# Kernel optimization log

Hardware: AMD Instinct MI355X
Metric: run time of the kernel (lower is better)

## Reference

```python
import jax, jax.numpy as jnp
import numpy as np

PATCH, STRIDE, NUM_PROJ, NBINS = 7, 1, 16, 2 ** 16
B, C, H, W = 2, 3, 384, 384


def gaussian_kernel(size=7, sigma=1.2):
    x = jnp.arange(size, dtype=jnp.float32)
    # faithful to original: exp(...)**2 (square applied OUTSIDE the exp)
    return jnp.exp((x - size // 2) ** 2 / (-2.0 * sigma ** 2)) ** 2


def extract_patches(img, p, s):
    # Equivalent of F.unfold: [b, c, h, w] -> [b, N, c*p*p], torch channel-major feature order
    b, c, h, w = img.shape
    Ho = (h - p) // s + 1
    Wo = (w - p) // s + 1
    cols = [img[:, :, i:i + (Ho - 1) * s + 1:s, j:j + (Wo - 1) * s + 1:s]
            for i in range(p) for j in range(p)]
    pat = jnp.stack(cols, axis=2)  # [b, c, p*p, Ho, Wo]
    return pat.reshape(b, c * p * p, Ho * Wo).transpose(0, 2, 1)  # [b, N, c*p*p]


def hist_distance(px, py):
    # px, py: [N] projected values for one (batch, projection) pair
    min_v = jnp.minimum(py.min(), px.min())
    max_v = jnp.maximum(py.max(), px.max())
    scale = max_v - min_v
    # scatter-set 1s into a 65536-bin histogram at data-dependent indices
    y_idx = jnp.floor((NBINS - 1) * (py - min_v) / scale).astype(jnp.int32)
    y_hist = jnp.zeros((NBINS,), jnp.float32).at[y_idx].set(1.0)
    # valid conv1d with 7-tap gaussian (symmetric kernel, so corr == conv)
    y_hist = jnp.convolve(y_hist, gaussian_kernel(), mode='valid')  # [NBINS-6]
    y_hist = jnp.minimum(y_hist, 1.0)
    Wd = y_hist.shape[0]
    # grid_sample (bilinear, align_corners=False, zero padding) on a 1-tall image == 1D linear interp
    gx = 2.0 * (px - min_v) / scale - 1.0
    ix = ((gx + 1.0) * Wd - 1.0) / 2.0
    x0 = jnp.floor(ix)
    w1 = ix - x0
    x0i = x0.astype(jnp.int32)
    x1i = x0i + 1
    v0 = jnp.where((x0i >= 0) & (x0i < Wd), y_hist[jnp.clip(x0i, 0, Wd - 1)], 0.0)
    v1 = jnp.where((x1i >= 0) & (x1i < Wd), y_hist[jnp.clip(x1i, 0, Wd - 1)], 0.0)
    return -(v0 * (1.0 - w1) + v1 * w1).sum()


def setup_inputs() -> dict:
    key = jax.random.key(0)
    k1, k2, k3 = jax.random.split(key, 3)
    x = jax.random.normal(k1, (B, C, H, W), dtype=jnp.float32)
    y = jax.random.normal(k2, (B, C, H, W), dtype=jnp.float32)
    rand = jax.random.normal(k3, (B, C * PATCH * PATCH, NUM_PROJ), dtype=jnp.float32)
    return {"x": x, "y": y, "rand": rand}


def reference(x, y, rand):
    xp = extract_patches(x, PATCH, STRIDE)  # [b, N, d]
    yp = extract_patches(y, PATCH, STRIDE)
    # torch.std(dim=0) is unbiased (ddof=1)
    r = rand / jnp.std(rand, axis=1, keepdims=True, ddof=1)  # [b, d, P]
    proj_x = jnp.einsum('bnd,bdp->bpn', xp, r)
    proj_y = jnp.einsum('bnd,bdp->bpn', yp, r)
    losses = jax.vmap(jax.vmap(hist_distance))(proj_x, proj_y)  # [b, P]
    per_image = losses.sum(axis=1) / NUM_PROJ
    return per_image.mean()  # batch_reduction='mean'
```

## Files before the change

### kernel.cpp

```cpp
#include <hip/hip_runtime.h>
#include <math.h>
#include <stdint.h>

#define NPROJ 16
#define NBINS 65536
#define WD (NBINS - 6)
#define HB 65560
#define B_ 2
#define C_ 3
#define H_ 384
#define W_ 384
#define HO 378
#define NPAT (HO * HO)
#define DF 147
#define BP 32
#define TSTR 24

__device__ inline unsigned f2key(float f) {
    unsigned u = __float_as_uint(f);
    return (u & 0x80000000u) ? ~u : (u | 0x80000000u);
}
__device__ inline float key2f(unsigned k) {
    unsigned u = (k & 0x80000000u) ? (k ^ 0x80000000u) : ~k;
    return __uint_as_float(u);
}

__global__ __launch_bounds__(64) void k_rnorm(const float* __restrict__ rnd,
                                              float* __restrict__ rnorm,
                                              unsigned* __restrict__ keys,
                                              float* __restrict__ out) {
    int bp = blockIdx.x;
    int b = bp / NPROJ, p = bp % NPROJ;
    int lane = threadIdx.x;
    if (lane == 0) {
        keys[2 * bp] = 0xFFFFFFFFu;
        keys[2 * bp + 1] = 0u;
        if (bp == 0) out[0] = 0.f;
    }
    float s = 0.f, s2 = 0.f;
    for (int d = lane; d < DF; d += 64) {
        float v = rnd[((size_t)b * DF + d) * NPROJ + p];
        s += v; s2 += v * v;
    }
    for (int o = 32; o > 0; o >>= 1) { s += __shfl_down(s, o); s2 += __shfl_down(s2, o); }
    s = __shfl(s, 0); s2 = __shfl(s2, 0);
    float mean = s / (float)DF;
    float var = (s2 - (float)DF * mean * mean) / (float)(DF - 1);
    float inv = 1.0f / sqrtf(var);
    for (int d = lane; d < DF; d += 64) {
        size_t idx = ((size_t)b * DF + d) * NPROJ + p;
        rnorm[idx] = rnd[idx] * inv;
    }
}

#define T1H 32
#define T1W 16
__global__ __launch_bounds__(256) void k_projmm(const float* __restrict__ ximg,
                                                const float* __restrict__ yimg,
                                                const float* __restrict__ rnorm,
                                                float* __restrict__ py,
                                                unsigned* __restrict__ keys) {
    __shared__ float tile[C_][T1H + 6][TSTR];
    __shared__ float red_mn[4][NPROJ], red_mx[4][NPROJ];
    int bz = blockIdx.z;
    int b = bz >> 1, isy = bz & 1;
    const float* img = isy ? yimg : ximg;
    int tid = threadIdx.x;
    int tx = tid & 15, ty = tid >> 4;
    int h0 = blockIdx.y * T1H, w0 = blockIdx.x * T1W;

    for (int c = 0; c < C_; c++)
        for (int i = tid; i < (T1H + 6) * (T1W + 6); i += 256) {
            int r = i / (T1W + 6), col = i % (T1W + 6);
            int h = h0 + r, w = w0 + col;
            tile[c][r][col] = (h < H_ && w < W_)
                ? img[((size_t)(b * C_ + c) * H_ + h) * W_ + w] : 0.f;
        }
    __syncthreads();

    const float* wbase = rnorm + (size_t)b * DF * NPROJ;

    float acc[2][NPROJ];
#pragma unroll
    for (int q = 0; q < 2; q++)
#pragma unroll
        for (int p = 0; p < NPROJ; p++) acc[q][p] = 0.f;

    for (int c = 0; c < C_; c++)
        for (int i = 0; i < 7; i++)
#pragma unroll
            for (int j = 0; j < 7; j++) {
                const float* wrow = wbase + (c * 49 + i * 7 + j) * NPROJ;
                float wv[NPROJ];
#pragma unroll
                for (int p = 0; p < NPROJ; p++) wv[p] = wrow[p];
                float pix0 = tile[c][ty + i][tx + j];
                float pix1 = tile[c][ty + 16 + i][tx + j];
#pragma unroll
                for (int p = 0; p < NPROJ; p++) {
                    acc[0][p] = fmaf(pix0, wv[p], acc[0][p]);
                    acc[1][p] = fmaf(pix1, wv[p], acc[1][p]);
                }
            }

    int wo = w0 + tx;
    int ho0 = h0 + ty, ho1 = h0 + ty + 16;
    bool vm0 = (ho0 < HO) && (wo < HO);
    bool vm1 = (ho1 < HO) && (wo < HO);

    if (isy) {
        if (vm0) {
            size_t n = (size_t)ho0 * HO + wo;
#pragma unroll
            for (int p = 0; p < NPROJ; p++)
                py[((size_t)(b * NPROJ + p)) * NPAT + n] = acc[0][p];
        }
        if (vm1) {
            size_t n = (size_t)ho1 * HO + wo;
#pragma unroll
            for (int p = 0; p < NPROJ; p++)
                py[((size_t)(b * NPROJ + p)) * NPAT + n] = acc[1][p];
        }
    }

    float pmn[NPROJ], pmx[NPROJ];
#pragma unroll
    for (int p = 0; p < NPROJ; p++) {
        float mn = INFINITY, mx = -INFINITY;
        if (vm0) { mn = acc[0][p]; mx = acc[0][p]; }
        if (vm1) { mn = fminf(mn, acc[1][p]); mx = fmaxf(mx, acc[1][p]); }
        pmn[p] = mn; pmx[p] = mx;
    }
#pragma unroll
    for (int o = 1; o < 64; o <<= 1) {
#pragma unroll
        for (int p = 0; p < NPROJ; p++) {
            pmn[p] = fminf(pmn[p], __shfl_xor(pmn[p], o));
            pmx[p] = fmaxf(pmx[p], __shfl_xor(pmx[p], o));
        }
    }
    int wv4 = tid >> 6;
    if ((tid & 63) == 0) {
#pragma unroll
        for (int p = 0; p < NPROJ; p++) { red_mn[wv4][p] = pmn[p]; red_mx[wv4][p] = pmx[p]; }
    }
    __syncthreads();
    if (tid < NPROJ) {
        float mn = fminf(fminf(red_mn[0][tid], red_mn[1][tid]),
                         fminf(red_mn[2][tid], red_mn[3][tid]));
        float mx = fmaxf(fmaxf(red_mx[0][tid], red_mx[1][tid]),
                         fmaxf(red_mx[2][tid], red_mx[3][tid]));
        atomicMin(&keys[2 * (b * NPROJ + tid)], f2key(mn));
        atomicMax(&keys[2 * (b * NPROJ + tid) + 1], f2key(mx));
    }
}

__global__ __launch_bounds__(256) void k_scatter(const float* __restrict__ py,
                                                 const unsigned* __restrict__ keys,
                                                 uint8_t* __restrict__ hist8) {
    int bp = blockIdx.y;
    float mn = key2f(keys[2 * bp]);
    float sc = key2f(keys[2 * bp + 1]) - mn;
    const float4* src = (const float4*)(py + (size_t)bp * NPAT);
    uint8_t* h = hist8 + (size_t)bp * HB + 8;
    const int n4 = NPAT / 4;
    for (int i = blockIdx.x * blockDim.x + threadIdx.x; i < n4;
         i += gridDim.x * blockDim.x) {
        float4 v = src[i];
        int i0 = (int)floorf(65535.f * (v.x - mn) / sc);
        int i1 = (int)floorf(65535.f * (v.y - mn) / sc);
        int i2 = (int)floorf(65535.f * (v.z - mn) / sc);
        int i3 = (int)floorf(65535.f * (v.w - mn) / sc);
        h[min(max(i0, 0), 65535)] = 1;
        h[min(max(i1, 0), 65535)] = 1;
        h[min(max(i2, 0), 65535)] = 1;
        h[min(max(i3, 0), 65535)] = 1;
    }
}

#define T3 16
__global__ __launch_bounds__(256) void k_projgather(const float* __restrict__ ximg,
                                                    const float* __restrict__ rnorm,
                                                    const unsigned* __restrict__ keys,
                                                    const uint8_t* __restrict__ hist8,
                                                    float* __restrict__ out) {
    __shared__ float tile[C_][T3 + 6][TSTR];
    __shared__ float s_mn[NPROJ], s_sc[NPROJ];
    __shared__ float sred[4];
    int b = blockIdx.z;
    int tid = threadIdx.x;
    int tx = tid & 15, ty = tid >> 4;
    int h0 = blockIdx.y * T3, w0 = blockIdx.x * T3;

    if (tid < NPROJ) {
        float mn = key2f(keys[2 * (b * NPROJ + tid)]);
        float mx = key2f(keys[2 * (b * NPROJ + tid) + 1]);
        s_mn[tid] = mn;
        s_sc[tid] = mx - mn;
    }
    for (int c = 0; c < C_; c++)
        for (int i = tid; i < (T3 + 6) * (T3 + 6); i += 256) {
            int r = i / (T3 + 6), col = i % (T3 + 6);
            int h = h0 + r, w = w0 + col;
            tile[c][r][col] = (h < H_ && w < W_)
                ? ximg[((size_t)(b * C_ + c) * H_ + h) * W_ + w] : 0.f;
        }
    __syncthreads();

    const float* wbase = rnorm + (size_t)b * DF * NPROJ;

    float acc[NPROJ];
#pragma unroll
    for (int p = 0; p < NPROJ; p++) acc[p] = 0.f;

    for (int c = 0; c < C_; c++)
        for (int i = 0; i < 7; i++)
#pragma unroll
            for (int j = 0; j < 7; j++) {
                const float* wrow = wbase + (c * 49 + i * 7 + j) * NPROJ;
                float wv[NPROJ];
#pragma unroll
                for (int p = 0; p < NPROJ; p++) wv[p] = wrow[p];
                float pix = tile[c][ty + i][tx + j];
#pragma unroll
                for (int p = 0; p < NPROJ; p++)
                    acc[p] = fmaf(pix, wv[p], acc[p]);
            }

    float g[7];
#pragma unroll
    for (int k = 0; k < 7; k++) {
        float d = (float)(k - 3);
        g[k] = expf(-(d * d) / 1.44f);
    }

    int wo = w0 + tx, ho = h0 + ty;
    float lacc = 0.f;
    if (ho < HO && wo < HO) {
#pragma unroll
        for (int p = 0; p < NPROJ; p++) {
            float v = acc[p];
            float t = (v - s_mn[p]) / s_sc[p];
            float ix = t * (float)WD - 0.5f;
            float x0 = floorf(ix);
            float w1 = ix - x0;
            int x0i = (int)x0;
            int b0 = 8 + x0i;
            int d0 = b0 >> 2, off = b0 & 3;
            const uint32_t* hw =
                (const uint32_t*)(hist8 + (size_t)(b * NPROJ + p) * HB);
            uint32_t u0 = hw[d0], u1 = hw[d0 + 1], u2 = hw[d0 + 2];
            uint64_t lo = (uint64_t)u0 | ((uint64_t)u1 << 32);
            int sh = off * 8;
            uint64_t w8 = (lo >> sh) | ((((uint64_t)u2) << 1) << (63 - sh));
            float f0 = (float)((uint32_t)(w8      ) & 1u);
            float f1 = (float)((uint32_t)(w8 >>  8) & 1u);
            float f2 = (float)((uint32_t)(w8 >> 16) & 1u);
            float f3 = (float)((uint32_t)(w8 >> 24) & 1u);
            float f4 = (float)((uint32_t)(w8 >> 32) & 1u);
            float f5 = (float)((uint32_t)(w8 >> 40) & 1u);
            float f6 = (float)((uint32_t)(w8 >> 48) & 1u);
            float f7 = (float)((uint32_t)(w8 >> 56) & 1u);
            float s0 = g[0] * f0 + g[1] * f1 + g[2] * f2 + g[3] * f3
                     + g[4] * f4 + g[5] * f5 + g[6] * f6;
            float s1 = g[0] * f1 + g[1] * f2 + g[2] * f3 + g[3] * f4
                     + g[4] * f5 + g[5] * f6 + g[6] * f7;
            s0 = fminf(s0, 1.f);
            s1 = fminf(s1, 1.f);
            float r0 = (x0i >= 0) ? s0 : 0.f;
            float r1 = (x0i + 1 < WD) ? s1 : 0.f;
            lacc += r0 * (1.f - w1) + r1 * w1;
        }
    }
    for (int o = 32; o > 0; o >>= 1) lacc += __shfl_down(lacc, o);
    int wv4 = tid >> 6;
    if ((tid & 63) == 0) sred[wv4] = lacc;
    __syncthreads();
    if (tid == 0) {
        float t = sred[0] + sred[1] + sred[2] + sred[3];
        atomicAdd(out, -t * (1.0f / 32.0f));
    }
}

extern "C" void kernel_launch(void* const* d_in, const int* in_sizes, int n_in,
                              void* d_out, int out_size, void* d_ws, size_t ws_size,
                              hipStream_t stream) {
    (void)in_sizes; (void)n_in; (void)out_size; (void)ws_size;
    const float* x = (const float*)d_in[0];
    const float* y = (const float*)d_in[1];
    const float* rnd = (const float*)d_in[2];
    float* out = (float*)d_out;

    float* ws = (float*)d_ws;
    float* rnorm = ws;
    float* py = rnorm + (size_t)B_ * DF * NPROJ;
    unsigned* keys = (unsigned*)(py + (size_t)BP * NPAT);
    uint8_t* hist8 = (uint8_t*)(keys + 2 * BP);

    k_rnorm<<<BP, 64, 0, stream>>>(rnd, rnorm, keys, out);
    hipMemsetAsync(hist8, 0, (size_t)BP * HB, stream);

    dim3 g1(384 / T1W, 384 / T1H, 2 * B_);
    k_projmm<<<g1, 256, 0, stream>>>(x, y, rnorm, py, keys);

    k_scatter<<<dim3(70, BP), 256, 0, stream>>>(py, keys, hist8);

    dim3 g3(384 / T3, 384 / T3, B_);
    k_projgather<<<g3, 256, 0, stream>>>(x, rnorm, keys, hist8, out);
}
```

Baseline: 119.9 us.

## Store x projections once and gather per projection instead of recomputing them

The projection kernel now writes the x projections to workspace along with the y projections, and uses 16x16 tiles with one output per thread. The final kernel no longer recomputes the 147x16 patch projection for x. It streams the stored values per (batch, projection) and looks up a single histogram each, which keeps that histogram's accesses local in cache. The cost is an extra ~9 MB write and read of x projections, and smaller projection tiles, which reduce weight reuse.

```diff
diff --git a/kernel.cpp b/kernel.cpp
--- a/kernel.cpp
+++ b/kernel.cpp
@@ -53,25 +53,26 @@
     }
 }
 
-#define T1H 32
-#define T1W 16
+#define T1 16
 __global__ __launch_bounds__(256) void k_projmm(const float* __restrict__ ximg,
                                                 const float* __restrict__ yimg,
                                                 const float* __restrict__ rnorm,
+                                                float* __restrict__ px,
                                                 float* __restrict__ py,
                                                 unsigned* __restrict__ keys) {
-    __shared__ float tile[C_][T1H + 6][TSTR];
+    __shared__ float tile[C_][T1 + 6][TSTR];
     __shared__ float red_mn[4][NPROJ], red_mx[4][NPROJ];
     int bz = blockIdx.z;
     int b = bz >> 1, isy = bz & 1;
     const float* img = isy ? yimg : ximg;
+    float* proj = isy ? py : px;
     int tid = threadIdx.x;
     int tx = tid & 15, ty = tid >> 4;
-    int h0 = blockIdx.y * T1H, w0 = blockIdx.x * T1W;
+    int h0 = blockIdx.y * T1, w0 = blockIdx.x * T1;
 
     for (int c = 0; c < C_; c++)
-        for (int i = tid; i < (T1H + 6) * (T1W + 6); i += 256) {
-            int r = i / (T1W + 6), col = i % (T1W + 6);
+        for (int i = tid; i < (T1 + 6) * (T1 + 6); i += 256) {
+            int r = i / (T1 + 6), col = i % (T1 + 6);
             int h = h0 + r, w = w0 + col;
             tile[c][r][col] = (h < H_ && w < W_)
                 ? img[((size_t)(b * C_ + c) * H_ + h) * W_ + w] : 0.f;
@@ -80,11 +81,9 @@
 
     const float* wbase = rnorm + (size_t)b * DF * NPROJ;
 
-    float acc[2][NPROJ];
-#pragma unroll
-    for (int q = 0; q < 2; q++)
-#pragma unroll
-        for (int p = 0; p < NPROJ; p++) acc[q][p] = 0.f;
+    float acc[NPROJ];
+#pragma unroll
+    for (int p = 0; p < NPROJ; p++) acc[p] = 0.f;
 
     for (int c = 0; c < C_; c++)
         for (int i = 0; i < 7; i++)
@@ -94,42 +93,27 @@
                 float wv[NPROJ];
 #pragma unroll
                 for (int p = 0; p < NPROJ; p++) wv[p] = wrow[p];
-                float pix0 = tile[c][ty + i][tx + j];
-                float pix1 = tile[c][ty + 16 + i][tx + j];
-#pragma unroll
-                for (int p = 0; p < NPROJ; p++) {
-                    acc[0][p] = fmaf(pix0, wv[p], acc[0][p]);
-                    acc[1][p] = fmaf(pix1, wv[p], acc[1][p]);
-                }
+                float pix = tile[c][ty + i][tx + j];
+#pragma unroll
+                for (int p = 0; p < NPROJ; p++)
+                    acc[p] = fmaf(pix, wv[p], acc[p]);
             }
 
-    int wo = w0 + tx;
-    int ho0 = h0 + ty, ho1 = h0 + ty + 16;
-    bool vm0 = (ho0 < HO) && (wo < HO);
-    bool vm1 = (ho1 < HO) && (wo < HO);
-
-    if (isy) {
-        if (vm0) {
-            size_t n = (size_t)ho0 * HO + wo;
-#pragma unroll
-            for (int p = 0; p < NPROJ; p++)
-                py[((size_t)(b * NPROJ + p)) * NPAT + n] = acc[0][p];
-        }
-        if (vm1) {
-            size_t n = (size_t)ho1 * HO + wo;
-#pragma unroll
-            for (int p = 0; p < NPROJ; p++)
-                py[((size_t)(b * NPROJ + p)) * NPAT + n] = acc[1][p];
-        }
+    int wo = w0 + tx, ho = h0 + ty;
+    bool vm = (ho < HO) && (wo < HO);
+
+    if (vm) {
+        size_t n = (size_t)ho * HO + wo;
+#pragma unroll
+        for (int p = 0; p < NPROJ; p++)
+            proj[((size_t)(b * NPROJ + p)) * NPAT + n] = acc[p];
     }
 
     float pmn[NPROJ], pmx[NPROJ];
 #pragma unroll
     for (int p = 0; p < NPROJ; p++) {
-        float mn = INFINITY, mx = -INFINITY;
-        if (vm0) { mn = acc[0][p]; mx = acc[0][p]; }
-        if (vm1) { mn = fminf(mn, acc[1][p]); mx = fmaxf(mx, acc[1][p]); }
-        pmn[p] = mn; pmx[p] = mx;
+        pmn[p] = vm ? acc[p] : INFINITY;
+        pmx[p] = vm ? acc[p] : -INFINITY;
     }
 #pragma unroll
     for (int o = 1; o < 64; o <<= 1) {
@@ -178,105 +162,69 @@
     }
 }
 
-#define T3 16
-__global__ __launch_bounds__(256) void k_projgather(const float* __restrict__ ximg,
-                                                    const float* __restrict__ rnorm,
-                                                    const unsigned* __restrict__ keys,
-                                                    const uint8_t* __restrict__ hist8,
-                                                    float* __restrict__ out) {
-    __shared__ float tile[C_][T3 + 6][TSTR];
-    __shared__ float s_mn[NPROJ], s_sc[NPROJ];
-    __shared__ float sred[4];
-    int b = blockIdx.z;
-    int tid = threadIdx.x;
-    int tx = tid & 15, ty = tid >> 4;
-    int h0 = blockIdx.y * T3, w0 = blockIdx.x * T3;
-
-    if (tid < NPROJ) {
-        float mn = key2f(keys[2 * (b * NPROJ + tid)]);
-        float mx = key2f(keys[2 * (b * NPROJ + tid) + 1]);
-        s_mn[tid] = mn;
-        s_sc[tid] = mx - mn;
-    }
-    for (int c = 0; c < C_; c++)
-        for (int i = tid; i < (T3 + 6) * (T3 + 6); i += 256) {
-            int r = i / (T3 + 6), col = i % (T3 + 6);
-            int h = h0 + r, w = w0 + col;
-            tile[c][r][col] = (h < H_ && w < W_)
-                ? ximg[((size_t)(b * C_ + c) * H_ + h) * W_ + w] : 0.f;
-        }
-    __syncthreads();
-
-    const float* wbase = rnorm + (size_t)b * DF * NPROJ;
-
-    float acc[NPROJ];
-#pragma unroll
-    for (int p = 0; p < NPROJ; p++) acc[p] = 0.f;
-
-    for (int c = 0; c < C_; c++)
-        for (int i = 0; i < 7; i++)
-#pragma unroll
-            for (int j = 0; j < 7; j++) {
-                const float* wrow = wbase + (c * 49 + i * 7 + j) * NPROJ;
-                float wv[NPROJ];
-#pragma unroll
-                for (int p = 0; p < NPROJ; p++) wv[p] = wrow[p];
-                float pix = tile[c][ty + i][tx + j];
-#pragma unroll
-                for (int p = 0; p < NPROJ; p++)
-                    acc[p] = fmaf(pix, wv[p], acc[p]);
-            }
-
+__device__ inline float gath8(const uint32_t* __restrict__ hw, float v,
+                              float mn, float sc, const float g[7]) {
+    float t = (v - mn) / sc;
+    float ix = t * (float)WD - 0.5f;
+    float x0 = floorf(ix);
+    float w1 = ix - x0;
+    int x0i = (int)x0;
+    int b0 = 8 + x0i;
+    int d0 = b0 >> 2, off = b0 & 3;
+    uint32_t u0 = hw[d0], u1 = hw[d0 + 1], u2 = hw[d0 + 2];
+    uint64_t lo = (uint64_t)u0 | ((uint64_t)u1 << 32);
+    int sh = off * 8;
+    uint64_t w8 = (lo >> sh) | ((((uint64_t)u2) << 1) << (63 - sh));
+    float f0 = (float)((uint32_t)(w8      ) & 1u);
+    float f1 = (float)((uint32_t)(w8 >>  8) & 1u);
+    float f2 = (float)((uint32_t)(w8 >> 16) & 1u);
+    float f3 = (float)((uint32_t)(w8 >> 24) & 1u);
+    float f4 = (float)((uint32_t)(w8 >> 32) & 1u);
+    float f5 = (float)((uint32_t)(w8 >> 40) & 1u);
+    float f6 = (float)((uint32_t)(w8 >> 48) & 1u);
+    float f7 = (float)((uint32_t)(w8 >> 56) & 1u);
+    float s0 = g[0] * f0 + g[1] * f1 + g[2] * f2 + g[3] * f3
+             + g[4] * f4 + g[5] * f5 + g[6] * f6;
+    float s1 = g[0] * f1 + g[1] * f2 + g[2] * f3 + g[3] * f4
+             + g[4] * f5 + g[5] * f6 + g[6] * f7;
+    s0 = fminf(s0, 1.f);
+    s1 = fminf(s1, 1.f);
+    float r0 = (x0i >= 0) ? s0 : 0.f;
+    float r1 = (x0i + 1 < WD) ? s1 : 0.f;
+    return r0 * (1.f - w1) + r1 * w1;
+}
+
+__global__ __launch_bounds__(256) void k_gather8(const float* __restrict__ px,
+                                                 const unsigned* __restrict__ keys,
+                                                 const uint8_t* __restrict__ hist8,
+                                                 float* __restrict__ out) {
+    int bp = blockIdx.y;
+    float mn = key2f(keys[2 * bp]);
+    float sc = key2f(keys[2 * bp + 1]) - mn;
+    const float4* src = (const float4*)(px + (size_t)bp * NPAT);
+    const uint32_t* hw = (const uint32_t*)(hist8 + (size_t)bp * HB);
     float g[7];
 #pragma unroll
     for (int k = 0; k < 7; k++) {
         float d = (float)(k - 3);
         g[k] = expf(-(d * d) / 1.44f);
     }
-
-    int wo = w0 + tx, ho = h0 + ty;
-    float lacc = 0.f;
-    if (ho < HO && wo < HO) {
-#pragma unroll
-        for (int p = 0; p < NPROJ; p++) {
-            float v = acc[p];
-            float t = (v - s_mn[p]) / s_sc[p];
-            float ix = t * (float)WD - 0.5f;
-            float x0 = floorf(ix);
-            float w1 = ix - x0;
-            int x0i = (int)x0;
-            int b0 = 8 + x0i;
-            int d0 = b0 >> 2, off = b0 & 3;
-            const uint32_t* hw =
-                (const uint32_t*)(hist8 + (size_t)(b * NPROJ + p) * HB);
-            uint32_t u0 = hw[d0], u1 = hw[d0 + 1], u2 = hw[d0 + 2];
-            uint64_t lo = (uint64_t)u0 | ((uint64_t)u1 << 32);
-            int sh = off * 8;
-            uint64_t w8 = (lo >> sh) | ((((uint64_t)u2) << 1) << (63 - sh));
-            float f0 = (float)((uint32_t)(w8      ) & 1u);
-            float f1 = (float)((uint32_t)(w8 >>  8) & 1u);
-            float f2 = (float)((uint32_t)(w8 >> 16) & 1u);
-            float f3 = (float)((uint32_t)(w8 >> 24) & 1u);
-            float f4 = (float)((uint32_t)(w8 >> 32) & 1u);
-            float f5 = (float)((uint32_t)(w8 >> 40) & 1u);
-            float f6 = (float)((uint32_t)(w8 >> 48) & 1u);
-            float f7 = (float)((uint32_t)(w8 >> 56) & 1u);
-            float s0 = g[0] * f0 + g[1] * f1 + g[2] * f2 + g[3] * f3
-                     + g[4] * f4 + g[5] * f5 + g[6] * f6;
-            float s1 = g[0] * f1 + g[1] * f2 + g[2] * f3 + g[3] * f4
-                     + g[4] * f5 + g[5] * f6 + g[6] * f7;
-            s0 = fminf(s0, 1.f);
-            s1 = fminf(s1, 1.f);
-            float r0 = (x0i >= 0) ? s0 : 0.f;
-            float r1 = (x0i + 1 < WD) ? s1 : 0.f;
-            lacc += r0 * (1.f - w1) + r1 * w1;
-        }
-    }
-    for (int o = 32; o > 0; o >>= 1) lacc += __shfl_down(lacc, o);
-    int wv4 = tid >> 6;
-    if ((tid & 63) == 0) sred[wv4] = lacc;
+    float acc = 0.f;
+    const int n4 = NPAT / 4;
+    for (int i = blockIdx.x * blockDim.x + threadIdx.x; i < n4;
+         i += gridDim.x * blockDim.x) {
+        float4 v = src[i];
+        acc += gath8(hw, v.x, mn, sc, g);
+        acc += gath8(hw, v.y, mn, sc, g);
+        acc += gath8(hw, v.z, mn, sc, g);
+        acc += gath8(hw, v.w, mn, sc, g);
+    }
+    for (int o = 32; o > 0; o >>= 1) acc += __shfl_down(acc, o);
+    __shared__ float sred[4];
+    int wv4 = threadIdx.x >> 6;
+    if ((threadIdx.x & 63) == 0) sred[wv4] = acc;
     __syncthreads();
-    if (tid == 0) {
+    if (threadIdx.x == 0) {
         float t = sred[0] + sred[1] + sred[2] + sred[3];
         atomicAdd(out, -t * (1.0f / 32.0f));
     }
@@ -293,18 +241,18 @@
 
     float* ws = (float*)d_ws;
     float* rnorm = ws;
-    float* py = rnorm + (size_t)B_ * DF * NPROJ;
+    float* px = rnorm + (size_t)B_ * DF * NPROJ;
+    float* py = px + (size_t)BP * NPAT;
     unsigned* keys = (unsigned*)(py + (size_t)BP * NPAT);
     uint8_t* hist8 = (uint8_t*)(keys + 2 * BP);
 
     k_rnorm<<<BP, 64, 0, stream>>>(rnd, rnorm, keys, out);
     hipMemsetAsync(hist8, 0, (size_t)BP * HB, stream);
 
-    dim3 g1(384 / T1W, 384 / T1H, 2 * B_);
-    k_projmm<<<g1, 256, 0, stream>>>(x, y, rnorm, py, keys);
+    dim3 g1(384 / T1, 384 / T1, 2 * B_);
+    k_projmm<<<g1, 256, 0, stream>>>(x, y, rnorm, px, py, keys);
 
     k_scatter<<<dim3(70, BP), 256, 0, stream>>>(py, keys, hist8);
 
-    dim3 g3(384 / T3, 384 / T3, B_);
-    k_projgather<<<g3, 256, 0, stream>>>(x, rnorm, keys, hist8, out);
-}
+    k_gather8<<<dim3(70, BP), 256, 0, stream>>>(px, keys, hist8, out);
+}
```

Measured after the change: 137.3 us. 14.6% more time.

## Store x projections, compress histogram to bitmap, gather via LUT

Applied to the files above, without the earlier changes.

Instead of recomputing the x patch projection inside the gather kernel, the projection kernel now writes x projections to workspace as well. A new compress kernel packs the byte histogram into a bitmap, and a new gather kernel streams the stored projections and looks up each 8-bit window in a 256-entry shared-memory table of precomputed clamped convolution sums. The aim is to drop the redundant 147x16 FMA recompute and the per-sample 7-tap convolution, and to shrink the gather's random-access footprint. The cost is extra global write and read traffic for the x projections (about 9 MB) plus one more kernel launch.

```diff
diff --git a/kernel.cpp b/kernel.cpp
--- a/kernel.cpp
+++ b/kernel.cpp
@@ -5,7 +5,8 @@
 #define NPROJ 16
 #define NBINS 65536
 #define WD (NBINS - 6)
-#define HB 65560
+#define HB 65792
+#define BMW 2056
 #define B_ 2
 #define C_ 3
 #define H_ 384
@@ -58,6 +59,7 @@
 __global__ __launch_bounds__(256) void k_projmm(const float* __restrict__ ximg,
                                                 const float* __restrict__ yimg,
                                                 const float* __restrict__ rnorm,
+                                                float* __restrict__ px,
                                                 float* __restrict__ py,
                                                 unsigned* __restrict__ keys) {
     __shared__ float tile[C_][T1H + 6][TSTR];
@@ -65,6 +67,7 @@
     int bz = blockIdx.z;
     int b = bz >> 1, isy = bz & 1;
     const float* img = isy ? yimg : ximg;
+    float* proj = isy ? py : px;
     int tid = threadIdx.x;
     int tx = tid & 15, ty = tid >> 4;
     int h0 = blockIdx.y * T1H, w0 = blockIdx.x * T1W;
@@ -108,19 +111,17 @@
     bool vm0 = (ho0 < HO) && (wo < HO);
     bool vm1 = (ho1 < HO) && (wo < HO);
 
-    if (isy) {
-        if (vm0) {
-            size_t n = (size_t)ho0 * HO + wo;
-#pragma unroll
-            for (int p = 0; p < NPROJ; p++)
-                py[((size_t)(b * NPROJ + p)) * NPAT + n] = acc[0][p];
-        }
-        if (vm1) {
-            size_t n = (size_t)ho1 * HO + wo;
-#pragma unroll
-            for (int p = 0; p < NPROJ; p++)
-                py[((size_t)(b * NPROJ + p)) * NPAT + n] = acc[1][p];
-        }
+    if (vm0) {
+        size_t n = (size_t)ho0 * HO + wo;
+#pragma unroll
+        for (int p = 0; p < NPROJ; p++)
+            proj[((size_t)(b * NPROJ + p)) * NPAT + n] = acc[0][p];
+    }
+    if (vm1) {
+        size_t n = (size_t)ho1 * HO + wo;
+#pragma unroll
+        for (int p = 0; p < NPROJ; p++)
+            proj[((size_t)(b * NPROJ + p)) * NPAT + n] = acc[1][p];
     }
 
     float pmn[NPROJ], pmx[NPROJ];
@@ -178,54 +179,34 @@
     }
 }
 
-#define T3 16
-__global__ __launch_bounds__(256) void k_projgather(const float* __restrict__ ximg,
-                                                    const float* __restrict__ rnorm,
-                                                    const unsigned* __restrict__ keys,
-                                                    const uint8_t* __restrict__ hist8,
-                                                    float* __restrict__ out) {
-    __shared__ float tile[C_][T3 + 6][TSTR];
-    __shared__ float s_mn[NPROJ], s_sc[NPROJ];
+__global__ __launch_bounds__(256) void k_compress(const uint8_t* __restrict__ hist8,
+                                                  uint32_t* __restrict__ bitmap) {
+    int bp = blockIdx.y;
+    const uint8_t* src = hist8 + (size_t)bp * HB;
+    uint32_t* dst = bitmap + (size_t)bp * BMW;
+    for (int d = blockIdx.x * blockDim.x + threadIdx.x; d < BMW;
+         d += gridDim.x * blockDim.x) {
+        const uint4* s = (const uint4*)(src + 32 * d);
+        uint4 a = s[0], b = s[1];
+        uint32_t u[8] = { a.x, a.y, a.z, a.w, b.x, b.y, b.z, b.w };
+        uint32_t w = 0;
+#pragma unroll
+        for (int k = 0; k < 8; k++) {
+            uint32_t nib = (u[k] | (u[k] >> 7) | (u[k] >> 14) | (u[k] >> 21)) & 0xFu;
+            w |= nib << (4 * k);
+        }
+        dst[d] = w;
+    }
+}
+
+__global__ __launch_bounds__(256) void k_gather(const float* __restrict__ px,
+                                                const unsigned* __restrict__ keys,
+                                                const uint32_t* __restrict__ bitmap,
+                                                float* __restrict__ out) {
+    __shared__ float2 lut[256];
     __shared__ float sred[4];
-    int b = blockIdx.z;
+    int bp = blockIdx.y;
     int tid = threadIdx.x;
-    int tx = tid & 15, ty = tid >> 4;
-    int h0 = blockIdx.y * T3, w0 = blockIdx.x * T3;
-
-    if (tid < NPROJ) {
-        float mn = key2f(keys[2 * (b * NPROJ + tid)]);
-        float mx = key2f(keys[2 * (b * NPROJ + tid) + 1]);
-        s_mn[tid] = mn;
-        s_sc[tid] = mx - mn;
-    }
-    for (int c = 0; c < C_; c++)
-        for (int i = tid; i < (T3 + 6) * (T3 + 6); i += 256) {
-            int r = i / (T3 + 6), col = i % (T3 + 6);
-            int h = h0 + r, w = w0 + col;
-            tile[c][r][col] = (h < H_ && w < W_)
-                ? ximg[((size_t)(b * C_ + c) * H_ + h) * W_ + w] : 0.f;
-        }
-    __syncthreads();
-
-    const float* wbase = rnorm + (size_t)b * DF * NPROJ;
-
-    float acc[NPROJ];
-#pragma unroll
-    for (int p = 0; p < NPROJ; p++) acc[p] = 0.f;
-
-    for (int c = 0; c < C_; c++)
-        for (int i = 0; i < 7; i++)
-#pragma unroll
-            for (int j = 0; j < 7; j++) {
-                const float* wrow = wbase + (c * 49 + i * 7 + j) * NPROJ;
-                float wv[NPROJ];
-#pragma unroll
-                for (int p = 0; p < NPROJ; p++) wv[p] = wrow[p];
-                float pix = tile[c][ty + i][tx + j];
-#pragma unroll
-                for (int p = 0; p < NPROJ; p++)
-                    acc[p] = fmaf(pix, wv[p], acc[p]);
-            }
 
     float g[7];
 #pragma unroll
@@ -233,48 +214,51 @@
         float d = (float)(k - 3);
         g[k] = expf(-(d * d) / 1.44f);
     }
-
-    int wo = w0 + tx, ho = h0 + ty;
-    float lacc = 0.f;
-    if (ho < HO && wo < HO) {
-#pragma unroll
-        for (int p = 0; p < NPROJ; p++) {
-            float v = acc[p];
-            float t = (v - s_mn[p]) / s_sc[p];
+    {
+        int m = tid;
+        float f[8];
+#pragma unroll
+        for (int k = 0; k < 8; k++) f[k] = (float)((m >> k) & 1);
+        float s0 = g[0] * f[0] + g[1] * f[1] + g[2] * f[2] + g[3] * f[3]
+                 + g[4] * f[4] + g[5] * f[5] + g[6] * f[6];
+        float s1 = g[0] * f[1] + g[1] * f[2] + g[2] * f[3] + g[3] * f[4]
+                 + g[4] * f[5] + g[5] * f[6] + g[6] * f[7];
+        lut[m] = make_float2(fminf(s0, 1.f), fminf(s1, 1.f));
+    }
+    __syncthreads();
+
+    float mn = key2f(keys[2 * bp]);
+    float sc = key2f(keys[2 * bp + 1]) - mn;
+    const float4* src = (const float4*)(px + (size_t)bp * NPAT);
+    const uint8_t* bm = (const uint8_t*)(bitmap + (size_t)bp * BMW);
+
+    float acc = 0.f;
+    const int n4 = NPAT / 4;
+    for (int i = blockIdx.x * blockDim.x + threadIdx.x; i < n4;
+         i += gridDim.x * blockDim.x) {
+        float4 v4 = src[i];
+        float vv[4] = { v4.x, v4.y, v4.z, v4.w };
+#pragma unroll
+        for (int j = 0; j < 4; j++) {
+            float v = vv[j];
+            float t = (v - mn) / sc;
             float ix = t * (float)WD - 0.5f;
             float x0 = floorf(ix);
             float w1 = ix - x0;
             int x0i = (int)x0;
-            int b0 = 8 + x0i;
-            int d0 = b0 >> 2, off = b0 & 3;
-            const uint32_t* hw =
-                (const uint32_t*)(hist8 + (size_t)(b * NPROJ + p) * HB);
-            uint32_t u0 = hw[d0], u1 = hw[d0 + 1], u2 = hw[d0 + 2];
-            uint64_t lo = (uint64_t)u0 | ((uint64_t)u1 << 32);
-            int sh = off * 8;
-            uint64_t w8 = (lo >> sh) | ((((uint64_t)u2) << 1) << (63 - sh));
-            float f0 = (float)((uint32_t)(w8      ) & 1u);
-            float f1 = (float)((uint32_t)(w8 >>  8) & 1u);
-            float f2 = (float)((uint32_t)(w8 >> 16) & 1u);
-            float f3 = (float)((uint32_t)(w8 >> 24) & 1u);
-            float f4 = (float)((uint32_t)(w8 >> 32) & 1u);
-            float f5 = (float)((uint32_t)(w8 >> 40) & 1u);
-            float f6 = (float)((uint32_t)(w8 >> 48) & 1u);
-            float f7 = (float)((uint32_t)(w8 >> 56) & 1u);
-            float s0 = g[0] * f0 + g[1] * f1 + g[2] * f2 + g[3] * f3
-                     + g[4] * f4 + g[5] * f5 + g[6] * f6;
-            float s1 = g[0] * f1 + g[1] * f2 + g[2] * f3 + g[3] * f4
-                     + g[4] * f5 + g[5] * f6 + g[6] * f7;
-            s0 = fminf(s0, 1.f);
-            s1 = fminf(s1, 1.f);
-            float r0 = (x0i >= 0) ? s0 : 0.f;
-            float r1 = (x0i + 1 < WD) ? s1 : 0.f;
-            lacc += r0 * (1.f - w1) + r1 * w1;
-        }
-    }
-    for (int o = 32; o > 0; o >>= 1) lacc += __shfl_down(lacc, o);
+            int bit0 = 8 + x0i;
+            uint32_t u;
+            __builtin_memcpy(&u, bm + 2 * (bit0 >> 4), 4);
+            uint32_t w8 = (u >> (bit0 & 15)) & 0xFFu;
+            float2 sv = lut[w8];
+            float r0 = (x0i >= 0) ? sv.x : 0.f;
+            float r1 = (x0i + 1 < WD) ? sv.y : 0.f;
+            acc += r0 * (1.f - w1) + r1 * w1;
+        }
+    }
+    for (int o = 32; o > 0; o >>= 1) acc += __shfl_down(acc, o);
     int wv4 = tid >> 6;
-    if ((tid & 63) == 0) sred[wv4] = lacc;
+    if ((tid & 63) == 0) sred[wv4] = acc;
     __syncthreads();
     if (tid == 0) {
         float t = sred[0] + sred[1] + sred[2] + sred[3];
@@ -293,18 +277,19 @@
 
     float* ws = (float*)d_ws;
     float* rnorm = ws;
-    float* py = rnorm + (size_t)B_ * DF * NPROJ;
+    float* px = rnorm + (size_t)B_ * DF * NPROJ;
+    float* py = px + (size_t)BP * NPAT;
     unsigned* keys = (unsigned*)(py + (size_t)BP * NPAT);
     uint8_t* hist8 = (uint8_t*)(keys + 2 * BP);
+    uint32_t* bitmap = (uint32_t*)(hist8 + (size_t)BP * HB);
 
     k_rnorm<<<BP, 64, 0, stream>>>(rnd, rnorm, keys, out);
     hipMemsetAsync(hist8, 0, (size_t)BP * HB, stream);
 
     dim3 g1(384 / T1W, 384 / T1H, 2 * B_);
-    k_projmm<<<g1, 256, 0, stream>>>(x, y, rnorm, py, keys);
+    k_projmm<<<g1, 256, 0, stream>>>(x, y, rnorm, px, py, keys);
 
     k_scatter<<<dim3(70, BP), 256, 0, stream>>>(py, keys, hist8);
-
-    dim3 g3(384 / T3, 384 / T3, B_);
-    k_projgather<<<g3, 256, 0, stream>>>(x, rnorm, keys, hist8, out);
-}
+    k_compress<<<dim3(9, BP), 256, 0, stream>>>(hist8, bitmap);
+    k_gather<<<dim3(70, BP), 256, 0, stream>>>(px, keys, bitmap, out);
+}
```

Measured after the change: 121.0 us. About the same (+1.0%).
